# Performance work log

Hardware: AMD Instinct MI355X
Metric: run time of the kernel (lower is better)

Reference implementation:

```python
import jax, jax.numpy as jnp
import numpy as np

EPS = 1e-5

def gn(x, w, b):
    # torch GroupNorm(num_groups=1, C) on [N, C]: normalize over channels per row
    m = jnp.mean(x, axis=-1, keepdims=True)
    v = jnp.mean((x - m) ** 2, axis=-1, keepdims=True)
    return (x - m) * jax.lax.rsqrt(v + EPS) * w + b

def att_layer(agts, ctr_d, hi, wi, nodes, p):
    (Wd1, bd1, Wd2, gnd2_w, gnd2_b, Wq, gnq_w, gnq_b,
     Wc1, gnc1_w, gnc1_b, Wc2, Wa, gnn_w, gnn_b, Wl, gnl_w, gnl_b) = p
    res = agts
    # dist MLP on edge ctr differences [E,2]
    d = jax.nn.relu(ctr_d @ Wd1.T + bd1)                     # [E, n_ctx]
    d = jax.nn.relu(gn(d @ Wd2.T, gnd2_w, gnd2_b))           # [E, n_ctx]
    # query from gathered actor features
    q = jax.nn.relu(gn(agts[hi] @ Wq.T, gnq_w, gnq_b))       # [E, n_ctx]
    # context: concat(dist, query, gathered lane feats) -> MLP
    cf = jnp.concatenate([d, q, nodes[wi]], axis=-1)         # [E, 3*n_ctx]
    cf = jax.nn.relu(gn(cf @ Wc1.T, gnc1_w, gnc1_b))         # [E, n_agt]
    cf = cf @ Wc2.T                                          # [E, n_agt]
    # scatter-aggregate onto actors
    a = agts @ Wa.T
    a = a.at[hi].add(cf)
    a = jax.nn.relu(gn(a, gnn_w, gnn_b))
    a = gn(a @ Wl.T, gnl_w, gnl_b)  # Linear with act=False
    return jax.nn.relu(a + res)

def setup_inputs() -> dict:
    key = jax.random.key(0)
    ks = jax.random.split(key, 20)
    M, N, E, D = 4000, 20000, 150000, 128
    s2 = 1.0 / np.sqrt(2.0)
    s128 = 1.0 / np.sqrt(128.0)
    s384 = 1.0 / np.sqrt(384.0)
    inp = {}
    inp["actors"] = jax.random.normal(ks[0], (M, D), jnp.float32)
    inp["nodes"] = jax.random.normal(ks[1], (N, D), jnp.float32)
    inp["actor_ctrs"] = jax.random.uniform(ks[2], (M, 2), jnp.float32)
    inp["node_ctrs"] = jax.random.uniform(ks[3], (N, 2), jnp.float32)
    inp["hi"] = jax.random.randint(ks[4], (E,), 0, M, dtype=jnp.int32)
    inp["wi"] = jax.random.randint(ks[5], (E,), 0, N, dtype=jnp.int32)
    inp["Wd1"] = jax.random.normal(ks[6], (2, D, 2), jnp.float32) * s2
    inp["bd1"] = jnp.zeros((2, D), jnp.float32)
    inp["Wd2"] = jax.random.normal(ks[7], (2, D, D), jnp.float32) * s128
    inp["gnd2_w"] = jnp.ones((2, D), jnp.float32)
    inp["gnd2_b"] = jnp.zeros((2, D), jnp.float32)
    inp["Wq"] = jax.random.normal(ks[8], (2, D, D), jnp.float32) * s128
    inp["gnq_w"] = jnp.ones((2, D), jnp.float32)
    inp["gnq_b"] = jnp.zeros((2, D), jnp.float32)
    inp["Wc1"] = jax.random.normal(ks[9], (2, D, 3 * D), jnp.float32) * s384
    inp["gnc1_w"] = jnp.ones((2, D), jnp.float32)
    inp["gnc1_b"] = jnp.zeros((2, D), jnp.float32)
    inp["Wc2"] = jax.random.normal(ks[10], (2, D, D), jnp.float32) * s128
    inp["Wa"] = jax.random.normal(ks[11], (2, D, D), jnp.float32) * s128
    inp["gnn_w"] = jnp.ones((2, D), jnp.float32)
    inp["gnn_b"] = jnp.zeros((2, D), jnp.float32)
    inp["Wl"] = jax.random.normal(ks[12], (2, D, D), jnp.float32) * s128
    inp["gnl_w"] = jnp.ones((2, D), jnp.float32)
    inp["gnl_b"] = jnp.zeros((2, D), jnp.float32)
    return inp

def reference(actors, nodes, actor_ctrs, node_ctrs, hi, wi,
              Wd1, bd1, Wd2, gnd2_w, gnd2_b, Wq, gnq_w, gnq_b,
              Wc1, gnc1_w, gnc1_b, Wc2, Wa, gnn_w, gnn_b, Wl, gnl_w, gnl_b):
    ctr_d = actor_ctrs[hi] - node_ctrs[wi]  # [E, 2], same edges for both layers
    stacked = (Wd1, bd1, Wd2, gnd2_w, gnd2_b, Wq, gnq_w, gnq_b,
               Wc1, gnc1_w, gnc1_b, Wc2, Wa, gnn_w, gnn_b, Wl, gnl_w, gnl_b)
    agts = actors
    for i in range(2):  # two Att layers
        p = tuple(t[i] for t in stacked)
        agts = att_layer(agts, ctr_d, hi, wi, nodes, p)
    return agts
```

## Files before the change

### kernel.cpp

```cpp
#include <hip/hip_runtime.h>

#define M_ACT 4000
#define NNODE 20000
#define NE 150000
#define DD 128
#define NT_E 586
#define NB_N2 313
#define HB 587
#define AB 63
#define AB16 250
#define ASTR 136
#define WSTR 72
#define BSTR 136

typedef __attribute__((ext_vector_type(8))) short bh8;
typedef __attribute__((ext_vector_type(4))) float vf4;

#define MFMA16(a, b, c) __builtin_amdgcn_mfma_f32_16x16x32_bf16((a), (b), (c), 0, 0, 0)
#define LGKM0() __asm__ volatile("s_waitcnt lgkmcnt(0)" ::: "memory")

__device__ __forceinline__ unsigned short f2bf(float f) {
    unsigned u = __float_as_uint(f);
    u = (u + 0x7fffu + ((u >> 16) & 1u)) >> 16;
    return (unsigned short)u;
}
__device__ __forceinline__ float bf2f(unsigned short s) {
    return __uint_as_float(((unsigned)s) << 16);
}

__device__ __forceinline__ void gn_stats8(const vf4* acc, float* mean, float* rs) {
    float s[4], q[4];
#pragma unroll
    for (int i = 0; i < 4; i++) {
        float a = 0.f, b = 0.f;
#pragma unroll
        for (int t = 0; t < 8; t++) { float v = acc[t][i]; a += v; b += v * v; }
        s[i] = a; q[i] = b;
    }
#pragma unroll
    for (int m = 1; m < 16; m <<= 1) {
#pragma unroll
        for (int i = 0; i < 4; i++) {
            s[i] += __shfl_xor(s[i], m, 64);
            q[i] += __shfl_xor(q[i], m, 64);
        }
    }
#pragma unroll
    for (int i = 0; i < 4; i++) {
        float mu = s[i] * (1.0f / 128.0f);
        float var = q[i] * (1.0f / 128.0f) - mu * mu;
        mean[i] = mu;
        rs[i] = rsqrtf(var + 1e-5f);
    }
}

template <bool RELU>
__device__ __forceinline__ void gn_to_lds(const vf4* acc, const float* __restrict__ gw,
                                          const float* __restrict__ gb, unsigned short* sm,
                                          int stride, int cb, int r0, int grp, int lm) {
    float mean[4], rs[4];
    gn_stats8(acc, mean, rs);
#pragma unroll
    for (int t = 0; t < 8; t++) {
        int c = 16 * t + lm;
        float w = gw[c], b = gb[c];
#pragma unroll
        for (int i = 0; i < 4; i++) {
            float y = (acc[t][i] - mean[i]) * rs[i] * w + b;
            if (RELU) y = fmaxf(y, 0.0f);
            sm[(r0 + grp * 4 + i) * stride + cb + c] = f2bf(y);
        }
    }
}

__device__ __forceinline__ void load_chunk(const unsigned short* __restrict__ src,
                                           unsigned short* dst, int tid) {
    for (int idx = tid; idx < 1152; idx += 256) {
        *(uint4*)&dst[idx * 8] = *(const uint4*)&src[idx * 8];
    }
}

__device__ __forceinline__ void gemm16(const unsigned short* smA,
                                       const unsigned short* __restrict__ w2ch, vf4* acc,
                                       int grp, int lm) {
#pragma unroll
    for (int ks = 0; ks < 4; ks++) {
        bh8 a = *(const bh8*)&smA[lm * ASTR + ks * 32 + grp * 8];
#pragma unroll
        for (int t = 0; t < 8; t++) {
            bh8 b = *(const bh8*)&w2ch[(ks >> 1) * 9216 + (16 * t + lm) * WSTR +
                                       (ks & 1) * 32 + grp * 8];
            acc[t] = MFMA16(a, b, acc[t]);
        }
    }
}

__device__ __forceinline__ void stage16(const float* __restrict__ src, int m0,
                                        unsigned short* smA, int lane) {
    for (int idx = lane; idx < 16 * 32; idx += 64) {
        int r = idx >> 5, q = idx & 31;
        const float4 v = *(const float4*)(src + (size_t)(m0 + r) * DD + q * 4);
        unsigned lo = (unsigned)f2bf(v.x) | ((unsigned)f2bf(v.y) << 16);
        unsigned hi2 = (unsigned)f2bf(v.z) | ((unsigned)f2bf(v.w) << 16);
        *(uint2*)&smA[r * ASTR + q * 4] = make_uint2(lo, hi2);
    }
}

__device__ __forceinline__ void q2_body(unsigned short* smA, unsigned short* smW,
                                        const unsigned short* __restrict__ wq,
                                        const unsigned short* __restrict__ wc,
                                        const float* __restrict__ gnq_w,
                                        const float* __restrict__ gnq_b,
                                        float* __restrict__ Q2, int m0, int tid) {
    const int wave = tid >> 6, lane = tid & 63, grp = lane >> 4, lm = lane & 15;
    const int r0 = wave * 16;
    const int arow = r0 + lm;
    vf4 acc[8];
#pragma unroll
    for (int t = 0; t < 8; t++) acc[t] = (vf4){0.f, 0.f, 0.f, 0.f};
    for (int ch = 0; ch < 2; ch++) {
        load_chunk(wq + ch * 9216, smW, tid);
        __syncthreads();
#pragma unroll
        for (int k0 = 0; k0 < 64; k0 += 32) {
            bh8 a = *(const bh8*)&smA[arow * ASTR + ch * 64 + k0 + grp * 8];
#pragma unroll
            for (int t = 0; t < 8; t++) {
                bh8 b = *(const bh8*)&smW[(16 * t + lm) * WSTR + k0 + grp * 8];
                acc[t] = MFMA16(a, b, acc[t]);
            }
        }
        __syncthreads();
    }
    gn_to_lds<true>(acc, gnq_w, gnq_b, smA, ASTR, 0, r0, grp, lm);

#pragma unroll
    for (int t = 0; t < 8; t++) acc[t] = (vf4){0.f, 0.f, 0.f, 0.f};
    for (int ch = 0; ch < 2; ch++) {
        load_chunk(wc + ch * 9216, smW, tid);
        __syncthreads();
#pragma unroll
        for (int k0 = 0; k0 < 64; k0 += 32) {
            bh8 a = *(const bh8*)&smA[arow * ASTR + ch * 64 + k0 + grp * 8];
#pragma unroll
            for (int t = 0; t < 8; t++) {
                bh8 b = *(const bh8*)&smW[(16 * t + lm) * WSTR + k0 + grp * 8];
                acc[t] = MFMA16(a, b, acc[t]);
            }
        }
        __syncthreads();
    }
#pragma unroll
    for (int t = 0; t < 8; t++) {
        int c = 16 * t + lm;
#pragma unroll
        for (int i = 0; i < 4; i++) {
            int m = m0 + r0 + grp * 4 + i;
            if (m < M_ACT) Q2[(size_t)m * DD + c] = acc[t][i];
        }
    }
}

__global__ void setup_kernel(const int* __restrict__ hi, int* __restrict__ hist,
                             const float* __restrict__ Wd2, const float* __restrict__ Wq,
                             const float* __restrict__ Wc1, const float* __restrict__ Wc2,
                             const float* __restrict__ Wa, const float* __restrict__ Wl,
                             unsigned short* __restrict__ wblob) {
    int b = blockIdx.x;
    if (b < HB) {
        int e = b * 256 + threadIdx.x;
        if (e < NE) atomicAdd(&hist[hi[e]], 1);
        return;
    }
    int ci = b - HB;
    int l = ci >> 4, r = ci & 15;
    const float* src;
    int kc, K;
    if (r < 2)       { src = Wd2 + l * 16384; kc = r;      K = 128; }
    else if (r < 4)  { src = Wq  + l * 16384; kc = r - 2;  K = 128; }
    else if (r < 10) { src = Wc1 + l * 49152; kc = r - 4;  K = 384; }
    else if (r < 12) { src = Wc2 + l * 16384; kc = r - 10; K = 128; }
    else if (r < 14) { src = Wa  + l * 16384; kc = r - 12; K = 128; }
    else             { src = Wl  + l * 16384; kc = r - 14; K = 128; }
    unsigned short* dst = wblob + (size_t)ci * 9216;
    for (int idx = threadIdx.x; idx < 9216; idx += 256) {
        int n = idx / 72, kk = idx - n * 72;
        float v = (kk < 64) ? src[n * K + kc * 64 + kk] : 0.f;
        dst[idx] = f2bf(v);
    }
}

__global__ void scan_kernel(const int* __restrict__ hist, int* __restrict__ cursor) {
    __shared__ int part[256];
    int t = threadIdx.x;
    int base = t * 16;
    int s = 0;
    if (base < M_ACT)
        for (int i = 0; i < 16; i++) s += hist[base + i];
    part[t] = s;
    __syncthreads();
    for (int d = 1; d < 256; d <<= 1) {
        int u = (t >= d) ? part[t - d] : 0;
        __syncthreads();
        part[t] += u;
        __syncthreads();
    }
    int excl = part[t] - s;
    if (base < M_ACT) {
        int run = excl;
        for (int i = 0; i < 16; i++) {
            cursor[base + i] = run;
            run += hist[base + i];
        }
    }
}

__global__ __launch_bounds__(256, 2) void mega0_kernel(
    const int* __restrict__ hi, const int* __restrict__ wi, int* __restrict__ cursor,
    int* __restrict__ hi_s, int* __restrict__ wi_s, const float* __restrict__ nodes,
    const unsigned short* __restrict__ wblob, float* __restrict__ N2_0,
    float* __restrict__ N2_1, const float* __restrict__ agts,
    const float* __restrict__ gnq_w, const float* __restrict__ gnq_b,
    float* __restrict__ Q2, float* __restrict__ Aa) {
    __shared__ unsigned short smA[64 * ASTR];
    __shared__ unsigned short smW[128 * WSTR];
    const int tid = threadIdx.x;
    int b = blockIdx.x;
    if (b < HB) {
        int e = b * 256 + tid;
        if (e < NE) {
            int h = hi[e];
            int p = atomicAdd(&cursor[h], 1);
            hi_s[p] = h;
            wi_s[p] = wi[e];
        }
        return;
    }
    b -= HB;
    const int wave = tid >> 6, lane = tid & 63, grp = lane >> 4, lm = lane & 15;
    const int r0 = wave * 16;
    const int arow = r0 + lm;
    if (b < 2 * NB_N2) {
        const int half = b / NB_N2;
        const int bx = b - half * NB_N2;
        const unsigned short* wblob_l = wblob + (size_t)half * 16 * 9216;
        float* __restrict__ N2 = half ? N2_1 : N2_0;
        const int n0 = bx * 64;
        for (int idx = tid; idx < 64 * 32; idx += 256) {
            int r = idx >> 5, q = idx & 31;
            int n = n0 + r;
            if (n >= NNODE) n = 0;
            const float4 v = *(const float4*)(nodes + (size_t)n * DD + q * 4);
            unsigned lo = (unsigned)f2bf(v.x) | ((unsigned)f2bf(v.y) << 16);
            unsigned hi2 = (unsigned)f2bf(v.z) | ((unsigned)f2bf(v.w) << 16);
            *(uint2*)&smA[r * ASTR + q * 4] = make_uint2(lo, hi2);
        }
        __syncthreads();
        vf4 acc[8];
#pragma unroll
        for (int t = 0; t < 8; t++) acc[t] = (vf4){0.f, 0.f, 0.f, 0.f};
        for (int ch = 0; ch < 2; ch++) {
            load_chunk(wblob_l + (8 + ch) * 9216, smW, tid);
            __syncthreads();
#pragma unroll
            for (int k0 = 0; k0 < 64; k0 += 32) {
                bh8 a = *(const bh8*)&smA[arow * ASTR + ch * 64 + k0 + grp * 8];
#pragma unroll
                for (int t = 0; t < 8; t++) {
                    bh8 bb = *(const bh8*)&smW[(16 * t + lm) * WSTR + k0 + grp * 8];
                    acc[t] = MFMA16(a, bb, acc[t]);
                }
            }
            __syncthreads();
        }
#pragma unroll
        for (int t = 0; t < 8; t++) {
            int c = 16 * t + lm;
#pragma unroll
            for (int i = 0; i < 4; i++) {
                int n = n0 + r0 + grp * 4 + i;
                if (n < NNODE) N2[(size_t)n * DD + c] = acc[t][i];
            }
        }
        return;
    }
    b -= 2 * NB_N2;
    const int m0 = (b < AB ? b : b - AB) * 64;
    for (int idx = tid; idx < 64 * 32; idx += 256) {
        int r = idx >> 5, q = idx & 31;
        int m = m0 + r;
        if (m >= M_ACT) m = 0;
        const float4 v = *(const float4*)(agts + (size_t)m * DD + q * 4);
        unsigned lo = (unsigned)f2bf(v.x) | ((unsigned)f2bf(v.y) << 16);
        unsigned hi2 = (unsigned)f2bf(v.z) | ((unsigned)f2bf(v.w) << 16);
        *(uint2*)&smA[r * ASTR + q * 4] = make_uint2(lo, hi2);
    }
    __syncthreads();
    if (b < AB) {
        q2_body(smA, smW, wblob + 2 * 9216, wblob + 6 * 9216, gnq_w, gnq_b, Q2, m0, tid);
        return;
    }
    vf4 acc[8];
#pragma unroll
    for (int t = 0; t < 8; t++) acc[t] = (vf4){0.f, 0.f, 0.f, 0.f};
    for (int ch = 0; ch < 2; ch++) {
        load_chunk(wblob + (12 + ch) * 9216, smW, tid);
        __syncthreads();
#pragma unroll
        for (int k0 = 0; k0 < 64; k0 += 32) {
            bh8 a = *(const bh8*)&smA[arow * ASTR + ch * 64 + k0 + grp * 8];
#pragma unroll
            for (int t = 0; t < 8; t++) {
                bh8 bb = *(const bh8*)&smW[(16 * t + lm) * WSTR + k0 + grp * 8];
                acc[t] = MFMA16(a, bb, acc[t]);
            }
        }
        __syncthreads();
    }
#pragma unroll
    for (int t = 0; t < 8; t++) {
        int c = 16 * t + lm;
#pragma unroll
        for (int i = 0; i < 4; i++) {
            int m = m0 + r0 + grp * 4 + i;
            if (m < M_ACT) Aa[(size_t)m * DD + c] = acc[t][i];
        }
    }
}

__global__ __launch_bounds__(512, 2) void edge_kernel(
    const float* __restrict__ actor_ctrs, const float* __restrict__ node_ctrs,
    const float* __restrict__ Wd1_l, const float* __restrict__ bd1_l,
    const float* __restrict__ Q2, const float* __restrict__ N2,
    const int* __restrict__ hi_s, const int* __restrict__ wi_s,
    const unsigned short* __restrict__ wblob_l,
    const float* __restrict__ gnd2_w, const float* __restrict__ gnd2_b,
    const float* __restrict__ gnc1_w, const float* __restrict__ gnc1_b,
    float* __restrict__ ssum, int* __restrict__ ctr) {
    __shared__ unsigned short smW[4 * 9216];
    __shared__ unsigned short smBuf[8][32 * BSTR];
    __shared__ float smWd1[3][128];
    __shared__ int smTile;
    {
        const int src0[4] = {0, 1, 4, 5};
#pragma unroll
        for (int s = 0; s < 4; s++)
            for (int idx = threadIdx.x; idx < 1152; idx += 512)
                *(uint4*)&smW[s * 9216 + idx * 8] =
                    *(const uint4*)&wblob_l[src0[s] * 9216 + idx * 8];
        for (int t = threadIdx.x; t < 128; t += 512) {
            smWd1[0][t] = Wd1_l[2 * t + 0];
            smWd1[1][t] = Wd1_l[2 * t + 1];
            smWd1[2][t] = bd1_l[t];
        }
    }
    const int wave = threadIdx.x >> 6, lane = threadIdx.x & 63;
    const int grp = lane >> 4, lm = lane & 15;
    unsigned short* buf = smBuf[wave];

    while (true) {
        __syncthreads();
        if (threadIdx.x == 0) smTile = atomicAdd(ctr, 1);
        __syncthreads();
        int tile = smTile;
        if (tile >= NT_E) break;
        int j0 = tile * 256 + wave * 32;
        if (j0 >= NE) continue;

        vf4 acc[2][8];
        int hg[2][4], wg[2][4];
        float cx[2], cy[2];
#pragma unroll
        for (int rt = 0; rt < 2; rt++) {
            int r = j0 + rt * 16 + lm;
            if (r > NE - 1) r = NE - 1;
            int hr = hi_s[r], wr = wi_s[r];
            cx[rt] = actor_ctrs[hr * 2 + 0] - node_ctrs[wr * 2 + 0];
            cy[rt] = actor_ctrs[hr * 2 + 1] - node_ctrs[wr * 2 + 1];
#pragma unroll
            for (int i = 0; i < 4; i++) {
                int j = j0 + rt * 16 + grp * 4 + i;
                if (j > NE - 1) j = NE - 1;
                hg[rt][i] = hi_s[j];
                wg[rt][i] = wi_s[j];
            }
        }
        bh8 a1[2][4];
#pragma unroll
        for (int ks = 0; ks < 4; ks++) {
            float wx[8], wy[8], wb[8];
#pragma unroll
            for (int e = 0; e < 8; e++) {
                int c = ks * 32 + grp * 8 + e;
                wx[e] = smWd1[0][c];
                wy[e] = smWd1[1][c];
                wb[e] = smWd1[2][c];
            }
#pragma unroll
            for (int rt = 0; rt < 2; rt++) {
                bh8 v;
#pragma unroll
                for (int e = 0; e < 8; e++) {
                    float x = fmaf(cy[rt], wy[e], fmaf(cx[rt], wx[e], wb[e]));
                    v[e] = (short)f2bf(fmaxf(x, 0.f));
                }
                a1[rt][ks] = v;
            }
        }
#pragma unroll
        for (int rt = 0; rt < 2; rt++)
#pragma unroll
            for (int t = 0; t < 8; t++) acc[rt][t] = (vf4){0.f, 0.f, 0.f, 0.f};
#pragma unroll
        for (int ks = 0; ks < 4; ks++) {
            bh8 B[8];
#pragma unroll
            for (int t = 0; t < 8; t++)
                B[t] = *(const bh8*)&smW[(ks >> 1) * 9216 + (16 * t + lm) * WSTR +
                                         (ks & 1) * 32 + grp * 8];
#pragma unroll
            for (int rt = 0; rt < 2; rt++)
#pragma unroll
                for (int t = 0; t < 8; t++) acc[rt][t] = MFMA16(a1[rt][ks], B[t], acc[rt][t]);
        }
        LGKM0();
#pragma unroll
        for (int rt = 0; rt < 2; rt++) {
            float mean[4], rs[4];
            gn_stats8(acc[rt], mean, rs);
#pragma unroll
            for (int t = 0; t < 8; t++) {
                int c = 16 * t + lm;
                float w = gnd2_w[c], b = gnd2_b[c];
#pragma unroll
                for (int i = 0; i < 4; i++) {
                    float y = (acc[rt][t][i] - mean[i]) * rs[i] * w + b;
                    buf[(rt * 16 + grp * 4 + i) * BSTR + c] = f2bf(fmaxf(y, 0.f));
                }
            }
        }
        LGKM0();
#pragma unroll
        for (int rt = 0; rt < 2; rt++)
#pragma unroll
            for (int t = 0; t < 8; t++) acc[rt][t] = (vf4){0.f, 0.f, 0.f, 0.f};
#pragma unroll
        for (int ks = 0; ks < 4; ks++) {
            bh8 B[8];
#pragma unroll
            for (int t = 0; t < 8; t++)
                B[t] = *(const bh8*)&smW[(2 + (ks >> 1)) * 9216 + (16 * t + lm) * WSTR +
                                         (ks & 1) * 32 + grp * 8];
#pragma unroll
            for (int rt = 0; rt < 2; rt++) {
                bh8 a = *(const bh8*)&buf[(rt * 16 + lm) * BSTR + ks * 32 + grp * 8];
#pragma unroll
                for (int t = 0; t < 8; t++) acc[rt][t] = MFMA16(a, B[t], acc[rt][t]);
            }
        }
#pragma unroll
        for (int rt = 0; rt < 2; rt++)
#pragma unroll
            for (int t = 0; t < 8; t++) {
                int c = 16 * t + lm;
#pragma unroll
                for (int i = 0; i < 4; i++)
                    acc[rt][t][i] +=
                        Q2[(size_t)hg[rt][i] * DD + c] + N2[(size_t)wg[rt][i] * DD + c];
            }
#pragma unroll
        for (int rt = 0; rt < 2; rt++) {
            float mean[4], rs[4];
            gn_stats8(acc[rt], mean, rs);
#pragma unroll
            for (int t = 0; t < 8; t++) {
                int c = 16 * t + lm;
                float w = gnc1_w[c], b = gnc1_b[c];
#pragma unroll
                for (int i = 0; i < 4; i++) {
                    float y = (acc[rt][t][i] - mean[i]) * rs[i] * w + b;
                    acc[rt][t][i] = fmaxf(y, 0.f);
                }
            }
        }
        {
            int hrem[2][4];
#pragma unroll
            for (int rt = 0; rt < 2; rt++)
#pragma unroll
                for (int i = 0; i < 4; i++) {
                    int j = j0 + rt * 16 + grp * 4 + i;
                    hrem[rt][i] = (j < NE) ? hg[rt][i] : -1;
                }
            while (true) {
                int hmin = 0x7fffffff;
#pragma unroll
                for (int rt = 0; rt < 2; rt++)
#pragma unroll
                    for (int i = 0; i < 4; i++)
                        if (hrem[rt][i] >= 0 && hrem[rt][i] < hmin) hmin = hrem[rt][i];
                hmin = min(hmin, __shfl_xor(hmin, 16, 64));
                hmin = min(hmin, __shfl_xor(hmin, 32, 64));
                if (hmin == 0x7fffffff) break;
                float p[8];
#pragma unroll
                for (int t = 0; t < 8; t++) p[t] = 0.f;
#pragma unroll
                for (int rt = 0; rt < 2; rt++)
#pragma unroll
                    for (int i = 0; i < 4; i++)
                        if (hrem[rt][i] == hmin) {
#pragma unroll
                            for (int t = 0; t < 8; t++) p[t] += acc[rt][t][i];
                            hrem[rt][i] = -1;
                        }
#pragma unroll
                for (int t = 0; t < 8; t++) {
                    p[t] += __shfl_xor(p[t], 16, 64);
                    p[t] += __shfl_xor(p[t], 32, 64);
                }
                if (grp == 0) {
#pragma unroll
                    for (int t = 0; t < 8; t++)
                        atomicAdd(&ssum[(size_t)hmin * DD + 16 * t + lm], p[t]);
                }
            }
        }
    }
}

__global__ __launch_bounds__(64) void actor_q2_kernel(
    const float* __restrict__ agts, const float* __restrict__ ssum,
    const float* __restrict__ Aa, const float* __restrict__ gnn_w,
    const float* __restrict__ gnn_b, const float* __restrict__ gnl_w,
    const float* __restrict__ gnl_b, const unsigned short* __restrict__ wblob,
    float* __restrict__ A1, const float* __restrict__ gnq_w1,
    const float* __restrict__ gnq_b1, float* __restrict__ Q2) {
    __shared__ unsigned short smA[16 * ASTR];
    const int lane = threadIdx.x, grp = lane >> 4, lm = lane & 15;
    const int m0 = blockIdx.x * 16;

    stage16(ssum, m0, smA, lane);
    __syncthreads();
    vf4 acc[8];
#pragma unroll
    for (int t = 0; t < 8; t++) acc[t] = (vf4){0.f, 0.f, 0.f, 0.f};
    gemm16(smA, wblob + 10 * 9216, acc, grp, lm);
#pragma unroll
    for (int t = 0; t < 8; t++) {
        int c = 16 * t + lm;
#pragma unroll
        for (int i = 0; i < 4; i++)
            acc[t][i] += Aa[(size_t)(m0 + grp * 4 + i) * DD + c];
    }
    __syncthreads();
    gn_to_lds<true>(acc, gnn_w, gnn_b, smA, ASTR, 0, 0, grp, lm);
    __syncthreads();
#pragma unroll
    for (int t = 0; t < 8; t++) acc[t] = (vf4){0.f, 0.f, 0.f, 0.f};
    gemm16(smA, wblob + 14 * 9216, acc, grp, lm);
    {
        float mean[4], rs[4];
        gn_stats8(acc, mean, rs);
        __syncthreads();
#pragma unroll
        for (int t = 0; t < 8; t++) {
            int c = 16 * t + lm;
            float w = gnl_w[c], b = gnl_b[c];
#pragma unroll
            for (int i = 0; i < 4; i++) {
                int m = m0 + grp * 4 + i;
                float y = (acc[t][i] - mean[i]) * rs[i] * w + b + agts[(size_t)m * DD + c];
                float o = fmaxf(y, 0.f);
                A1[(size_t)m * DD + c] = o;
                smA[(grp * 4 + i) * ASTR + c] = f2bf(o);
            }
        }
    }
    __syncthreads();
#pragma unroll
    for (int t = 0; t < 8; t++) acc[t] = (vf4){0.f, 0.f, 0.f, 0.f};
    gemm16(smA, wblob + (16 + 2) * 9216, acc, grp, lm);
    __syncthreads();
    gn_to_lds<true>(acc, gnq_w1, gnq_b1, smA, ASTR, 0, 0, grp, lm);
    __syncthreads();
#pragma unroll
    for (int t = 0; t < 8; t++) acc[t] = (vf4){0.f, 0.f, 0.f, 0.f};
    gemm16(smA, wblob + (16 + 6) * 9216, acc, grp, lm);
#pragma unroll
    for (int t = 0; t < 8; t++) {
        int c = 16 * t + lm;
#pragma unroll
        for (int i = 0; i < 4; i++)
            Q2[(size_t)(m0 + grp * 4 + i) * DD + c] = acc[t][i];
    }
}

__global__ __launch_bounds__(64) void actor_kernel(
    const float* __restrict__ A1, const float* __restrict__ ssum,
    const float* __restrict__ gnn_w, const float* __restrict__ gnn_b,
    const float* __restrict__ gnl_w, const float* __restrict__ gnl_b,
    const unsigned short* __restrict__ wblob_l, float* __restrict__ dst) {
    __shared__ unsigned short smA[16 * ASTR];
    const int lane = threadIdx.x, grp = lane >> 4, lm = lane & 15;
    const int m0 = blockIdx.x * 16;

    stage16(ssum, m0, smA, lane);
    __syncthreads();
    vf4 acc[8];
#pragma unroll
    for (int t = 0; t < 8; t++) acc[t] = (vf4){0.f, 0.f, 0.f, 0.f};
    gemm16(smA, wblob_l + 10 * 9216, acc, grp, lm);
    __syncthreads();
    stage16(A1, m0, smA, lane);
    __syncthreads();
    gemm16(smA, wblob_l + 12 * 9216, acc, grp, lm);
    __syncthreads();
    gn_to_lds<true>(acc, gnn_w, gnn_b, smA, ASTR, 0, 0, grp, lm);
    __syncthreads();
#pragma unroll
    for (int t = 0; t < 8; t++) acc[t] = (vf4){0.f, 0.f, 0.f, 0.f};
    gemm16(smA, wblob_l + 14 * 9216, acc, grp, lm);
    {
        float mean[4], rs[4];
        gn_stats8(acc, mean, rs);
#pragma unroll
        for (int t = 0; t < 8; t++) {
            int c = 16 * t + lm;
            float w = gnl_w[c], b = gnl_b[c];
#pragma unroll
            for (int i = 0; i < 4; i++) {
                int m = m0 + grp * 4 + i;
                float y = (acc[t][i] - mean[i]) * rs[i] * w + b + A1[(size_t)m * DD + c];
                dst[(size_t)m * DD + c] = fmaxf(y, 0.f);
            }
        }
    }
}

extern "C" void kernel_launch(void* const* d_in, const int* in_sizes, int n_in,
                              void* d_out, int out_size, void* d_ws, size_t ws_size,
                              hipStream_t stream) {
    const float* actors = (const float*)d_in[0];
    const float* nodes = (const float*)d_in[1];
    const float* actor_ctrs = (const float*)d_in[2];
    const float* node_ctrs = (const float*)d_in[3];
    const int* hi = (const int*)d_in[4];
    const int* wi = (const int*)d_in[5];
    const float* Wd1 = (const float*)d_in[6];
    const float* bd1 = (const float*)d_in[7];
    const float* Wd2 = (const float*)d_in[8];
    const float* gnd2_w = (const float*)d_in[9];
    const float* gnd2_b = (const float*)d_in[10];
    const float* Wq = (const float*)d_in[11];
    const float* gnq_w = (const float*)d_in[12];
    const float* gnq_b = (const float*)d_in[13];
    const float* Wc1 = (const float*)d_in[14];
    const float* gnc1_w = (const float*)d_in[15];
    const float* gnc1_b = (const float*)d_in[16];
    const float* Wc2 = (const float*)d_in[17];
    const float* Wa = (const float*)d_in[18];
    const float* gnn_w = (const float*)d_in[19];
    const float* gnn_b = (const float*)d_in[20];
    const float* Wl = (const float*)d_in[21];
    const float* gnl_w = (const float*)d_in[22];
    const float* gnl_b = (const float*)d_in[23];
    float* out = (float*)d_out;

    char* ws = (char*)d_ws;
    unsigned short* wblob = (unsigned short*)ws;  ws += 2 * 16 * 9216 * 2;
    float* Q2 = (float*)ws;                       ws += (size_t)M_ACT * DD * 4;
    float* N2_0 = (float*)ws;                     ws += (size_t)NNODE * DD * 4;
    float* N2_1 = (float*)ws;                     ws += (size_t)NNODE * DD * 4;
    float* A1 = (float*)ws;                       ws += (size_t)M_ACT * DD * 4;
    float* Aa = (float*)ws;                       ws += (size_t)M_ACT * DD * 4;
    int* cursor = (int*)ws;                       ws += M_ACT * 4;
    int* hi_s = (int*)ws;                         ws += NE * 4;
    int* wi_s = (int*)ws;                         ws += NE * 4;
    char* zbase = ws;
    int* hist = (int*)ws;                         ws += M_ACT * 4;
    int* ctr4 = (int*)ws;                         ws += 64;
    float* ssum0 = (float*)ws;                    ws += (size_t)M_ACT * DD * 4;
    float* ssum1 = (float*)ws;                    ws += (size_t)M_ACT * DD * 4;
    const size_t zbytes = (size_t)(ws - zbase);

    hipMemsetAsync(zbase, 0, zbytes, stream);
    setup_kernel<<<HB + 32, 256, 0, stream>>>(hi, hist, Wd2, Wq, Wc1, Wc2, Wa, Wl, wblob);
    scan_kernel<<<1, 256, 0, stream>>>(hist, cursor);

    const unsigned short* wb0 = wblob;
    const unsigned short* wb1 = wblob + 16 * 9216;

    mega0_kernel<<<HB + 2 * NB_N2 + 2 * AB, 256, 0, stream>>>(hi, wi, cursor, hi_s, wi_s,
                                                              nodes, wblob, N2_0, N2_1,
                                                              actors, gnq_w, gnq_b, Q2, Aa);
    edge_kernel<<<256, 512, 0, stream>>>(actor_ctrs, node_ctrs, Wd1, bd1, Q2, N2_0, hi_s,
                                         wi_s, wb0, gnd2_w, gnd2_b, gnc1_w, gnc1_b, ssum0,
                                         &ctr4[0]);
    actor_q2_kernel<<<AB16, 64, 0, stream>>>(actors, ssum0, Aa, gnn_w, gnn_b, gnl_w, gnl_b,
                                             wblob, A1, gnq_w + 128, gnq_b + 128, Q2);
    edge_kernel<<<256, 512, 0, stream>>>(actor_ctrs, node_ctrs, Wd1 + 256, bd1 + 128, Q2,
                                         N2_1, hi_s, wi_s, wb1, gnd2_w + 128, gnd2_b + 128,
                                         gnc1_w + 128, gnc1_b + 128, ssum1, &ctr4[1]);
    actor_kernel<<<AB16, 64, 0, stream>>>(A1, ssum1, gnn_w + 128, gnn_b + 128, gnl_w + 128,
                                          gnl_b + 128, wb1, out);
}
```

Measured before the change: 278.5 us.

## Redistribute precompute work across kernels to overlap with edge processing

Layer-0 actor Q2 and Aa projections move into the setup kernel, which converts the fp32 weights to bf16 on the fly instead of waiting for the packed weight blob. The layer-1 node projection N2_1 moves out of the pre-edge kernel into extra blocks of the first edge kernel, so it can run alongside the layer-0 edge work. The intent is to shorten the critical path by overlapping independent precompute with existing kernels. In exchange, weight conversion is repeated per block, and the appended edge-kernel blocks use a large LDS allocation that may limit co-residency.

```diff
diff --git a/kernel.cpp b/kernel.cpp
--- a/kernel.cpp
+++ b/kernel.cpp
@@ -80,6 +80,15 @@
     }
 }
 
+__device__ __forceinline__ void conv_chunk(const float* __restrict__ src, int K, int kc,
+                                           unsigned short* dst, int tid) {
+    for (int idx = tid; idx < 9216; idx += 256) {
+        int n = idx / 72, kk = idx - n * 72;
+        float v = (kk < 64) ? src[n * K + kc * 64 + kk] : 0.f;
+        dst[idx] = f2bf(v);
+    }
+}
+
 __device__ __forceinline__ void gemm16(const unsigned short* smA,
                                        const unsigned short* __restrict__ w2ch, vf4* acc,
                                        int grp, int lm) {
@@ -106,46 +115,113 @@
     }
 }
 
-__device__ __forceinline__ void q2_body(unsigned short* smA, unsigned short* smW,
-                                        const unsigned short* __restrict__ wq,
-                                        const unsigned short* __restrict__ wc,
-                                        const float* __restrict__ gnq_w,
-                                        const float* __restrict__ gnq_b,
-                                        float* __restrict__ Q2, int m0, int tid) {
+__global__ __launch_bounds__(256, 2) void setup_kernel(
+    const int* __restrict__ hi, int* __restrict__ hist, const float* __restrict__ Wd2,
+    const float* __restrict__ Wq, const float* __restrict__ Wc1,
+    const float* __restrict__ Wc2, const float* __restrict__ Wa,
+    const float* __restrict__ Wl, unsigned short* __restrict__ wblob,
+    const float* __restrict__ agts, const float* __restrict__ gnq_w,
+    const float* __restrict__ gnq_b, float* __restrict__ Q2, float* __restrict__ Aa) {
+    __shared__ unsigned short smA[64 * ASTR];
+    __shared__ unsigned short smW[128 * WSTR];
+    const int tid = threadIdx.x;
+    int b = blockIdx.x;
+    if (b < HB) {
+        int e = b * 256 + tid;
+        if (e < NE) atomicAdd(&hist[hi[e]], 1);
+        return;
+    }
+    b -= HB;
+    if (b < 32) {
+        int ci = b;
+        int l = ci >> 4, r = ci & 15;
+        const float* src;
+        int kc, K;
+        if (r < 2)       { src = Wd2 + l * 16384; kc = r;      K = 128; }
+        else if (r < 4)  { src = Wq  + l * 16384; kc = r - 2;  K = 128; }
+        else if (r < 10) { src = Wc1 + l * 49152; kc = r - 4;  K = 384; }
+        else if (r < 12) { src = Wc2 + l * 16384; kc = r - 10; K = 128; }
+        else if (r < 14) { src = Wa  + l * 16384; kc = r - 12; K = 128; }
+        else             { src = Wl  + l * 16384; kc = r - 14; K = 128; }
+        unsigned short* dst = wblob + (size_t)ci * 9216;
+        for (int idx = tid; idx < 9216; idx += 256) {
+            int n = idx / 72, kk = idx - n * 72;
+            float v = (kk < 64) ? src[n * K + kc * 64 + kk] : 0.f;
+            dst[idx] = f2bf(v);
+        }
+        return;
+    }
+    b -= 32;
     const int wave = tid >> 6, lane = tid & 63, grp = lane >> 4, lm = lane & 15;
     const int r0 = wave * 16;
     const int arow = r0 + lm;
+    const int m0 = (b < AB ? b : b - AB) * 64;
+    for (int idx = tid; idx < 64 * 32; idx += 256) {
+        int r = idx >> 5, q = idx & 31;
+        int m = m0 + r;
+        if (m >= M_ACT) m = 0;
+        const float4 v = *(const float4*)(agts + (size_t)m * DD + q * 4);
+        unsigned lo = (unsigned)f2bf(v.x) | ((unsigned)f2bf(v.y) << 16);
+        unsigned hi2 = (unsigned)f2bf(v.z) | ((unsigned)f2bf(v.w) << 16);
+        *(uint2*)&smA[r * ASTR + q * 4] = make_uint2(lo, hi2);
+    }
+    __syncthreads();
     vf4 acc[8];
 #pragma unroll
     for (int t = 0; t < 8; t++) acc[t] = (vf4){0.f, 0.f, 0.f, 0.f};
+    if (b < AB) {
+        for (int ch = 0; ch < 2; ch++) {
+            conv_chunk(Wq, 128, ch, smW, tid);
+            __syncthreads();
+#pragma unroll
+            for (int k0 = 0; k0 < 64; k0 += 32) {
+                bh8 a = *(const bh8*)&smA[arow * ASTR + ch * 64 + k0 + grp * 8];
+#pragma unroll
+                for (int t = 0; t < 8; t++) {
+                    bh8 bb = *(const bh8*)&smW[(16 * t + lm) * WSTR + k0 + grp * 8];
+                    acc[t] = MFMA16(a, bb, acc[t]);
+                }
+            }
+            __syncthreads();
+        }
+        gn_to_lds<true>(acc, gnq_w, gnq_b, smA, ASTR, 0, r0, grp, lm);
+#pragma unroll
+        for (int t = 0; t < 8; t++) acc[t] = (vf4){0.f, 0.f, 0.f, 0.f};
+        for (int ch = 0; ch < 2; ch++) {
+            conv_chunk(Wc1, 384, 2 + ch, smW, tid);
+            __syncthreads();
+#pragma unroll
+            for (int k0 = 0; k0 < 64; k0 += 32) {
+                bh8 a = *(const bh8*)&smA[arow * ASTR + ch * 64 + k0 + grp * 8];
+#pragma unroll
+                for (int t = 0; t < 8; t++) {
+                    bh8 bb = *(const bh8*)&smW[(16 * t + lm) * WSTR + k0 + grp * 8];
+                    acc[t] = MFMA16(a, bb, acc[t]);
+                }
+            }
+            __syncthreads();
+        }
+#pragma unroll
+        for (int t = 0; t < 8; t++) {
+            int c = 16 * t + lm;
+#pragma unroll
+            for (int i = 0; i < 4; i++) {
+                int m = m0 + r0 + grp * 4 + i;
+                if (m < M_ACT) Q2[(size_t)m * DD + c] = acc[t][i];
+            }
+        }
+        return;
+    }
     for (int ch = 0; ch < 2; ch++) {
-        load_chunk(wq + ch * 9216, smW, tid);
+        conv_chunk(Wa, 128, ch, smW, tid);
         __syncthreads();
 #pragma unroll
         for (int k0 = 0; k0 < 64; k0 += 32) {
             bh8 a = *(const bh8*)&smA[arow * ASTR + ch * 64 + k0 + grp * 8];
 #pragma unroll
             for (int t = 0; t < 8; t++) {
-                bh8 b = *(const bh8*)&smW[(16 * t + lm) * WSTR + k0 + grp * 8];
-                acc[t] = MFMA16(a, b, acc[t]);
-            }
-        }
-        __syncthreads();
-    }
-    gn_to_lds<true>(acc, gnq_w, gnq_b, smA, ASTR, 0, r0, grp, lm);
-
-#pragma unroll
-    for (int t = 0; t < 8; t++) acc[t] = (vf4){0.f, 0.f, 0.f, 0.f};
-    for (int ch = 0; ch < 2; ch++) {
-        load_chunk(wc + ch * 9216, smW, tid);
-        __syncthreads();
-#pragma unroll
-        for (int k0 = 0; k0 < 64; k0 += 32) {
-            bh8 a = *(const bh8*)&smA[arow * ASTR + ch * 64 + k0 + grp * 8];
-#pragma unroll
-            for (int t = 0; t < 8; t++) {
-                bh8 b = *(const bh8*)&smW[(16 * t + lm) * WSTR + k0 + grp * 8];
-                acc[t] = MFMA16(a, b, acc[t]);
+                bh8 bb = *(const bh8*)&smW[(16 * t + lm) * WSTR + k0 + grp * 8];
+                acc[t] = MFMA16(a, bb, acc[t]);
             }
         }
         __syncthreads();
@@ -156,37 +232,8 @@
 #pragma unroll
         for (int i = 0; i < 4; i++) {
             int m = m0 + r0 + grp * 4 + i;
-            if (m < M_ACT) Q2[(size_t)m * DD + c] = acc[t][i];
-        }
-    }
-}
-
-__global__ void setup_kernel(const int* __restrict__ hi, int* __restrict__ hist,
-                             const float* __restrict__ Wd2, const float* __restrict__ Wq,
-                             const float* __restrict__ Wc1, const float* __restrict__ Wc2,
-                             const float* __restrict__ Wa, const float* __restrict__ Wl,
-                             unsigned short* __restrict__ wblob) {
-    int b = blockIdx.x;
-    if (b < HB) {
-        int e = b * 256 + threadIdx.x;
-        if (e < NE) atomicAdd(&hist[hi[e]], 1);
-        return;
-    }
-    int ci = b - HB;
-    int l = ci >> 4, r = ci & 15;
-    const float* src;
-    int kc, K;
-    if (r < 2)       { src = Wd2 + l * 16384; kc = r;      K = 128; }
-    else if (r < 4)  { src = Wq  + l * 16384; kc = r - 2;  K = 128; }
-    else if (r < 10) { src = Wc1 + l * 49152; kc = r - 4;  K = 384; }
-    else if (r < 12) { src = Wc2 + l * 16384; kc = r - 10; K = 128; }
-    else if (r < 14) { src = Wa  + l * 16384; kc = r - 12; K = 128; }
-    else             { src = Wl  + l * 16384; kc = r - 14; K = 128; }
-    unsigned short* dst = wblob + (size_t)ci * 9216;
-    for (int idx = threadIdx.x; idx < 9216; idx += 256) {
-        int n = idx / 72, kk = idx - n * 72;
-        float v = (kk < 64) ? src[n * K + kc * 64 + kk] : 0.f;
-        dst[idx] = f2bf(v);
+            if (m < M_ACT) Aa[(size_t)m * DD + c] = acc[t][i];
+        }
     }
 }
 
@@ -215,13 +262,10 @@
     }
 }
 
-__global__ __launch_bounds__(256, 2) void mega0_kernel(
+__global__ __launch_bounds__(256, 2) void mega1_kernel(
     const int* __restrict__ hi, const int* __restrict__ wi, int* __restrict__ cursor,
     int* __restrict__ hi_s, int* __restrict__ wi_s, const float* __restrict__ nodes,
-    const unsigned short* __restrict__ wblob, float* __restrict__ N2_0,
-    float* __restrict__ N2_1, const float* __restrict__ agts,
-    const float* __restrict__ gnq_w, const float* __restrict__ gnq_b,
-    float* __restrict__ Q2, float* __restrict__ Aa) {
+    const unsigned short* __restrict__ wblob0, float* __restrict__ N2_0) {
     __shared__ unsigned short smA[64 * ASTR];
     __shared__ unsigned short smW[128 * WSTR];
     const int tid = threadIdx.x;
@@ -240,71 +284,22 @@
     const int wave = tid >> 6, lane = tid & 63, grp = lane >> 4, lm = lane & 15;
     const int r0 = wave * 16;
     const int arow = r0 + lm;
-    if (b < 2 * NB_N2) {
-        const int half = b / NB_N2;
-        const int bx = b - half * NB_N2;
-        const unsigned short* wblob_l = wblob + (size_t)half * 16 * 9216;
-        float* __restrict__ N2 = half ? N2_1 : N2_0;
-        const int n0 = bx * 64;
-        for (int idx = tid; idx < 64 * 32; idx += 256) {
-            int r = idx >> 5, q = idx & 31;
-            int n = n0 + r;
-            if (n >= NNODE) n = 0;
-            const float4 v = *(const float4*)(nodes + (size_t)n * DD + q * 4);
-            unsigned lo = (unsigned)f2bf(v.x) | ((unsigned)f2bf(v.y) << 16);
-            unsigned hi2 = (unsigned)f2bf(v.z) | ((unsigned)f2bf(v.w) << 16);
-            *(uint2*)&smA[r * ASTR + q * 4] = make_uint2(lo, hi2);
-        }
-        __syncthreads();
-        vf4 acc[8];
-#pragma unroll
-        for (int t = 0; t < 8; t++) acc[t] = (vf4){0.f, 0.f, 0.f, 0.f};
-        for (int ch = 0; ch < 2; ch++) {
-            load_chunk(wblob_l + (8 + ch) * 9216, smW, tid);
-            __syncthreads();
-#pragma unroll
-            for (int k0 = 0; k0 < 64; k0 += 32) {
-                bh8 a = *(const bh8*)&smA[arow * ASTR + ch * 64 + k0 + grp * 8];
-#pragma unroll
-                for (int t = 0; t < 8; t++) {
-                    bh8 bb = *(const bh8*)&smW[(16 * t + lm) * WSTR + k0 + grp * 8];
-                    acc[t] = MFMA16(a, bb, acc[t]);
-                }
-            }
-            __syncthreads();
-        }
-#pragma unroll
-        for (int t = 0; t < 8; t++) {
-            int c = 16 * t + lm;
-#pragma unroll
-            for (int i = 0; i < 4; i++) {
-                int n = n0 + r0 + grp * 4 + i;
-                if (n < NNODE) N2[(size_t)n * DD + c] = acc[t][i];
-            }
-        }
-        return;
-    }
-    b -= 2 * NB_N2;
-    const int m0 = (b < AB ? b : b - AB) * 64;
+    const int n0 = b * 64;
     for (int idx = tid; idx < 64 * 32; idx += 256) {
         int r = idx >> 5, q = idx & 31;
-        int m = m0 + r;
-        if (m >= M_ACT) m = 0;
-        const float4 v = *(const float4*)(agts + (size_t)m * DD + q * 4);
+        int n = n0 + r;
+        if (n >= NNODE) n = 0;
+        const float4 v = *(const float4*)(nodes + (size_t)n * DD + q * 4);
         unsigned lo = (unsigned)f2bf(v.x) | ((unsigned)f2bf(v.y) << 16);
         unsigned hi2 = (unsigned)f2bf(v.z) | ((unsigned)f2bf(v.w) << 16);
         *(uint2*)&smA[r * ASTR + q * 4] = make_uint2(lo, hi2);
     }
     __syncthreads();
-    if (b < AB) {
-        q2_body(smA, smW, wblob + 2 * 9216, wblob + 6 * 9216, gnq_w, gnq_b, Q2, m0, tid);
-        return;
-    }
     vf4 acc[8];
 #pragma unroll
     for (int t = 0; t < 8; t++) acc[t] = (vf4){0.f, 0.f, 0.f, 0.f};
     for (int ch = 0; ch < 2; ch++) {
-        load_chunk(wblob + (12 + ch) * 9216, smW, tid);
+        load_chunk(wblob0 + (8 + ch) * 9216, smW, tid);
         __syncthreads();
 #pragma unroll
         for (int k0 = 0; k0 < 64; k0 += 32) {
@@ -322,8 +317,8 @@
         int c = 16 * t + lm;
 #pragma unroll
         for (int i = 0; i < 4; i++) {
-            int m = m0 + r0 + grp * 4 + i;
-            if (m < M_ACT) Aa[(size_t)m * DD + c] = acc[t][i];
+            int n = n0 + r0 + grp * 4 + i;
+            if (n < NNODE) N2_0[(size_t)n * DD + c] = acc[t][i];
         }
     }
 }
@@ -336,11 +331,54 @@
     const unsigned short* __restrict__ wblob_l,
     const float* __restrict__ gnd2_w, const float* __restrict__ gnd2_b,
     const float* __restrict__ gnc1_w, const float* __restrict__ gnc1_b,
-    float* __restrict__ ssum, int* __restrict__ ctr) {
+    float* __restrict__ ssum, int* __restrict__ ctr, const float* __restrict__ nodes,
+    const unsigned short* __restrict__ wblob_n1, float* __restrict__ N2out) {
     __shared__ unsigned short smW[4 * 9216];
     __shared__ unsigned short smBuf[8][32 * BSTR];
     __shared__ float smWd1[3][128];
     __shared__ int smTile;
+    if (blockIdx.x >= 256) {
+        unsigned short* smA2 = &smBuf[0][0];
+        const int tid = threadIdx.x;
+        const int n0 = (blockIdx.x - 256) * 64;
+        for (int idx = tid; idx < 64 * 32; idx += 512) {
+            int r = idx >> 5, q = idx & 31;
+            int n = n0 + r;
+            if (n >= NNODE) n = 0;
+            const float4 v = *(const float4*)(nodes + (size_t)n * DD + q * 4);
+            unsigned lo = (unsigned)f2bf(v.x) | ((unsigned)f2bf(v.y) << 16);
+            unsigned hi2 = (unsigned)f2bf(v.z) | ((unsigned)f2bf(v.w) << 16);
+            *(uint2*)&smA2[r * BSTR + q * 4] = make_uint2(lo, hi2);
+        }
+        __syncthreads();
+        const int wv = tid >> 6, lane = tid & 63, grp = lane >> 4, lm = lane & 15;
+        const int rg = wv >> 1, th = wv & 1;
+        vf4 acc[4];
+#pragma unroll
+        for (int t = 0; t < 4; t++) acc[t] = (vf4){0.f, 0.f, 0.f, 0.f};
+#pragma unroll
+        for (int ks = 0; ks < 4; ks++) {
+            bh8 a = *(const bh8*)&smA2[(rg * 16 + lm) * BSTR + ks * 32 + grp * 8];
+#pragma unroll
+            for (int t = 0; t < 4; t++) {
+                int tt = th * 4 + t;
+                bh8 bb = *(const bh8*)&wblob_n1[(8 + (ks >> 1)) * 9216 +
+                                                (16 * tt + lm) * WSTR + (ks & 1) * 32 +
+                                                grp * 8];
+                acc[t] = MFMA16(a, bb, acc[t]);
+            }
+        }
+#pragma unroll
+        for (int t = 0; t < 4; t++) {
+            int c = 16 * (th * 4 + t) + lm;
+#pragma unroll
+            for (int i = 0; i < 4; i++) {
+                int n = n0 + rg * 16 + grp * 4 + i;
+                if (n < NNODE) N2out[(size_t)n * DD + c] = acc[t][i];
+            }
+        }
+        return;
+    }
     {
         const int src0[4] = {0, 1, 4, 5};
 #pragma unroll
@@ -684,24 +722,25 @@
     float* ssum1 = (float*)ws;                    ws += (size_t)M_ACT * DD * 4;
     const size_t zbytes = (size_t)(ws - zbase);
 
-    hipMemsetAsync(zbase, 0, zbytes, stream);
-    setup_kernel<<<HB + 32, 256, 0, stream>>>(hi, hist, Wd2, Wq, Wc1, Wc2, Wa, Wl, wblob);
+    (void)hipMemsetAsync(zbase, 0, zbytes, stream);
+    setup_kernel<<<HB + 32 + 2 * AB, 256, 0, stream>>>(hi, hist, Wd2, Wq, Wc1, Wc2, Wa, Wl,
+                                                       wblob, actors, gnq_w, gnq_b, Q2, Aa);
     scan_kernel<<<1, 256, 0, stream>>>(hist, cursor);
 
     const unsigned short* wb0 = wblob;
     const unsigned short* wb1 = wblob + 16 * 9216;
 
-    mega0_kernel<<<HB + 2 * NB_N2 + 2 * AB, 256, 0, stream>>>(hi, wi, cursor, hi_s, wi_s,
-                                                              nodes, wblob, N2_0, N2_1,
-                                                              actors, gnq_w, gnq_b, Q2, Aa);
-    edge_kernel<<<256, 512, 0, stream>>>(actor_ctrs, node_ctrs, Wd1, bd1, Q2, N2_0, hi_s,
-                                         wi_s, wb0, gnd2_w, gnd2_b, gnc1_w, gnc1_b, ssum0,
-                                         &ctr4[0]);
+    mega1_kernel<<<HB + NB_N2, 256, 0, stream>>>(hi, wi, cursor, hi_s, wi_s, nodes, wb0,
+                                                 N2_0);
+    edge_kernel<<<256 + NB_N2, 512, 0, stream>>>(actor_ctrs, node_ctrs, Wd1, bd1, Q2, N2_0,
+                                                 hi_s, wi_s, wb0, gnd2_w, gnd2_b, gnc1_w,
+                                                 gnc1_b, ssum0, &ctr4[0], nodes, wb1, N2_1);
     actor_q2_kernel<<<AB16, 64, 0, stream>>>(actors, ssum0, Aa, gnn_w, gnn_b, gnl_w, gnl_b,
                                              wblob, A1, gnq_w + 128, gnq_b + 128, Q2);
     edge_kernel<<<256, 512, 0, stream>>>(actor_ctrs, node_ctrs, Wd1 + 256, bd1 + 128, Q2,
                                          N2_1, hi_s, wi_s, wb1, gnd2_w + 128, gnd2_b + 128,
-                                         gnc1_w + 128, gnc1_b + 128, ssum1, &ctr4[1]);
+                                         gnc1_w + 128, gnc1_b + 128, ssum1, &ctr4[1], nodes,
+                                         wb1, N2_1);
     actor_kernel<<<AB16, 64, 0, stream>>>(A1, ssum1, gnn_w + 128, gnn_b + 128, gnl_w + 128,
                                           gnl_b + 128, wb1, out);
 }
```

Result: slower. 317.8 us (+14.1%).
